# Kernel tuning notes

Measured on AMD Instinct MI355X. Metric: run time of the kernel, lower is better.

Reference implementation:

```python
import jax, jax.numpy as jnp
import numpy as np

B, F, V, E, T, NTOK, G, D = 8192, 64, 1000, 64, 2, 16, 4, 256
LN_EPS = 1e-5


def setup_inputs() -> dict:
    key = jax.random.key(0)
    ks = jax.random.split(key, 5)
    int_feats = jax.random.randint(ks[0], (B, F), 0, V, dtype=jnp.int64)
    missing_mask = jax.random.randint(ks[1], (B, F), 0, 2, dtype=jnp.int32)
    # deterministic seeded permutation of features split into NTOK equal groups
    perm = np.random.default_rng(1234).permutation(F)
    group_idx = jnp.asarray(perm.reshape(NTOK, G), dtype=jnp.int32)
    emb_tables = jax.random.normal(ks[2], (T, F, V, E), jnp.float32) * 0.02
    missing_emb = jax.random.normal(ks[3], (T, F, E), jnp.float32) * 0.02
    kW, kb = jax.random.split(ks[4])
    W = jax.random.normal(kW, (D, E * T), jnp.float32) * (1.0 / np.sqrt(E * T))
    b = jnp.zeros((D,), jnp.float32)
    ln_gamma = jnp.ones((D,), jnp.float32)
    ln_beta = jnp.zeros((D,), jnp.float32)
    return {"int_feats": int_feats, "missing_mask": missing_mask,
            "group_idx": group_idx, "emb_tables": emb_tables,
            "missing_emb": missing_emb, "W": W, "b": b,
            "ln_gamma": ln_gamma, "ln_beta": ln_beta}


def reference(int_feats, missing_mask, group_idx, emb_tables, missing_emb, W, b, ln_gamma, ln_beta):
    f_idx = jnp.arange(F)[None, :]  # (1, F) broadcast with (B, F) ids
    # per-table feature embedding gather: [T, B, F, E]
    feats = jax.vmap(lambda tbl: tbl[f_idx, int_feats])(emb_tables)
    # additive missing embeddings
    mask = missing_mask.astype(feats.dtype)
    feats = feats + mask[None, :, :, None] * missing_emb[:, None, :, :]
    # token-group mean pooling: [T, B, NTOK, G, E] -> [T, B, NTOK, E]
    pooled = feats[:, :, group_idx, :].mean(axis=3)
    # concat tables along feature dim (table order preserved): [B, NTOK, T*E]
    x = jnp.moveaxis(pooled, 0, 2).reshape(B, NTOK, T * E)
    # Linear -> SiLU -> LayerNorm
    h = jax.nn.silu(x @ W.T + b)
    mu = h.mean(-1, keepdims=True)
    var = ((h - mu) ** 2).mean(-1, keepdims=True)
    return (h - mu) * jax.lax.rsqrt(var + LN_EPS) * ln_gamma + ln_beta
```

## Files before the change

### kernel.cpp

```cpp
#include <hip/hip_runtime.h>
#include <math.h>

#define B_    8192
#define F_    64
#define V_    1000
#define E_    64
#define T_    2
#define NTOK_ 16
#define G_    4
#define D_    256
#define K_    128
#define LN_EPS 1e-5f

#define XSP   136
#define HSP   260

typedef __attribute__((ext_vector_type(8))) short  frag_ab;
typedef __attribute__((ext_vector_type(4))) float  frag_cd;

static __device__ __forceinline__ unsigned short f2bf(float f) {
    unsigned int u = __float_as_uint(f);
    u += 0x7FFFu + ((u >> 16) & 1u);
    return (unsigned short)(u >> 16);
}

__global__ __launch_bounds__(256) void convert_w_kernel(const float* __restrict__ W,
                                                        unsigned int* __restrict__ Wb_packed) {
    const int i = blockIdx.x * 256 + threadIdx.x;
    if (i < (D_ * K_) / 2) {
        const float2 v = *(const float2*)(W + (size_t)i * 2);
        Wb_packed[i] = (unsigned int)f2bf(v.x) | ((unsigned int)f2bf(v.y) << 16);
    }
}

__global__ __launch_bounds__(256) void fused_tokenizer_kernel(
    const int*   __restrict__ int_feats,
    const int*   __restrict__ missing_mask,
    const int*   __restrict__ group_idx,
    const float* __restrict__ emb_tables,
    const float* __restrict__ missing_emb,
    const unsigned short* __restrict__ Wb,
    const float* __restrict__ bias,
    const float* __restrict__ gamma,
    const float* __restrict__ beta,
    float*       __restrict__ out)
{
    __shared__ unsigned short xs[NTOK_][XSP];
    __shared__ float          hs[NTOK_][HSP];
    __shared__ int   sid[F_];
    __shared__ int   smask[F_];
    __shared__ int   sg[NTOK_ * G_];

    const int tid  = threadIdx.x;
    const int b    = blockIdx.x;
    const int lane = tid & 63;
    const int wave = tid >> 6;

    if (tid < F_) {
        sid[tid]   = int_feats[b * F_ + tid];
        smask[tid] = missing_mask[b * F_ + tid];
        sg[tid]    = group_idx[tid];
    }
    __syncthreads();

#pragma unroll
    for (int i = 0; i < 2; ++i) {
        const int c  = i * 256 + tid;
        const int n  = c >> 5;
        const int r4 = c & 31;
        const int t  = r4 >> 4;
        const int e  = (r4 & 15) * 4;
        float ax = 0.f, ay = 0.f, az = 0.f, aw = 0.f;
#pragma unroll
        for (int g = 0; g < G_; ++g) {
            const int f  = sg[n * G_ + g];
            const int id = sid[f];
            const float4 v = *(const float4*)(emb_tables + (((size_t)(t * F_ + f) * V_) + id) * E_ + e);
            float vx = v.x, vy = v.y, vz = v.z, vw = v.w;
            if (smask[f]) {
                const float4 mv = *(const float4*)(missing_emb + (size_t)(t * F_ + f) * E_ + e);
                vx += mv.x; vy += mv.y; vz += mv.z; vw += mv.w;
            }
            ax += vx; ay += vy; az += vz; aw += vw;
        }
        union { unsigned int u[2]; } pk;
        pk.u[0] = (unsigned int)f2bf(0.25f * ax) | ((unsigned int)f2bf(0.25f * ay) << 16);
        pk.u[1] = (unsigned int)f2bf(0.25f * az) | ((unsigned int)f2bf(0.25f * aw) << 16);
        *(uint2*)(&xs[n][r4 * 4]) = make_uint2(pk.u[0], pk.u[1]);
    }
    __syncthreads();

    {
        const int mA = lane & 15;
        const int q  = lane >> 4;

        frag_ab a[4];
#pragma unroll
        for (int s = 0; s < 4; ++s)
            a[s] = *(const frag_ab*)(&xs[mA][32 * s + 8 * q]);

#pragma unroll
        for (int t = 0; t < 4; ++t) {
            const int nb   = wave * 64 + t * 16;
            const int nrow = nb + mA;
            const unsigned short* wp = Wb + (size_t)nrow * K_ + 8 * q;

            frag_cd acc = {0.f, 0.f, 0.f, 0.f};
#pragma unroll
            for (int s = 0; s < 4; ++s) {
                const frag_ab bfr = *(const frag_ab*)(wp + 32 * s);
                acc = __builtin_amdgcn_mfma_f32_16x16x32_bf16(a[s], bfr, acc, 0, 0, 0);
            }
            const float bn = bias[nrow];
#pragma unroll
            for (int reg = 0; reg < 4; ++reg) {
                const int tok = q * 4 + reg;
                const float z = acc[reg] + bn;
                hs[tok][nrow] = z / (1.f + __expf(-z));
            }
        }
    }
    __syncthreads();

    {
#pragma unroll
        for (int qq = 0; qq < 4; ++qq) {
            const int n = wave * 4 + qq;
            const float4 v = *(const float4*)(&hs[n][lane * 4]);
            float s  = v.x + v.y + v.z + v.w;
            float ss = v.x * v.x + v.y * v.y + v.z * v.z + v.w * v.w;
#pragma unroll
            for (int off = 32; off > 0; off >>= 1) {
                s  += __shfl_down(s,  off, 64);
                ss += __shfl_down(ss, off, 64);
            }
            s  = __shfl(s,  0, 64);
            ss = __shfl(ss, 0, 64);
            const float mu   = s * (1.f / D_);
            const float var  = ss * (1.f / D_) - mu * mu;
            const float rsig = rsqrtf(var + LN_EPS);

            const float4 gm = *(const float4*)(gamma + lane * 4);
            const float4 bt = *(const float4*)(beta  + lane * 4);
            float4 o;
            o.x = (v.x - mu) * rsig * gm.x + bt.x;
            o.y = (v.y - mu) * rsig * gm.y + bt.y;
            o.z = (v.z - mu) * rsig * gm.z + bt.z;
            o.w = (v.w - mu) * rsig * gm.w + bt.w;
            *(float4*)(out + ((size_t)b * NTOK_ + n) * D_ + lane * 4) = o;
        }
    }
}

extern "C" void kernel_launch(void* const* d_in, const int* in_sizes, int n_in,
                              void* d_out, int out_size, void* d_ws, size_t ws_size,
                              hipStream_t stream) {
    const int*   int_feats    = (const int*)  d_in[0];
    const int*   missing_mask = (const int*)  d_in[1];
    const int*   group_idx    = (const int*)  d_in[2];
    const float* emb_tables   = (const float*)d_in[3];
    const float* missing_emb  = (const float*)d_in[4];
    const float* W            = (const float*)d_in[5];
    const float* bias         = (const float*)d_in[6];
    const float* gamma        = (const float*)d_in[7];
    const float* beta         = (const float*)d_in[8];
    float* out = (float*)d_out;

    unsigned short* Wb = (unsigned short*)d_ws;

    convert_w_kernel<<<(D_ * K_ / 2 + 255) / 256, 256, 0, stream>>>(W, (unsigned int*)Wb);
    fused_tokenizer_kernel<<<B_, 256, 0, stream>>>(
        int_feats, missing_mask, group_idx, emb_tables, missing_emb,
        Wb, bias, gamma, beta, out);
}
```

Before: 242.6 us.

## Keep SiLU outputs in registers and fuse LayerNorm stats via swapped MFMA operands

The MFMA operands are swapped so each lane holds four consecutive output columns for one token. The SiLU outputs stay in registers, and per-token sum and sum-of-squares are reduced with cross-lane shuffles plus a tiny shared partial array. This removes the 16x256 float shared staging buffer and its extra pass. The index, mask and group staging into shared memory is also replaced by direct global loads, and the missing-embedding branch becomes an unconditional multiply-add. A leftover, incomplete copy of the old kernel is left in the file but is not launched.

```diff
diff --git a/kernel.cpp b/kernel.cpp
--- a/kernel.cpp
+++ b/kernel.cpp
@@ -13,7 +13,6 @@
 #define LN_EPS 1e-5f
 
 #define XSP   136
-#define HSP   260
 
 typedef __attribute__((ext_vector_type(8))) short  frag_ab;
 typedef __attribute__((ext_vector_type(4))) float  frag_cd;
@@ -46,22 +45,16 @@
     float*       __restrict__ out)
 {
     __shared__ unsigned short xs[NTOK_][XSP];
-    __shared__ float          hs[NTOK_][HSP];
-    __shared__ int   sid[F_];
-    __shared__ int   smask[F_];
-    __shared__ int   sg[NTOK_ * G_];
+    __shared__ float ps [NTOK_][4];
+    __shared__ float pss[NTOK_][4];
 
     const int tid  = threadIdx.x;
     const int b    = blockIdx.x;
     const int lane = tid & 63;
     const int wave = tid >> 6;
 
-    if (tid < F_) {
-        sid[tid]   = int_feats[b * F_ + tid];
-        smask[tid] = missing_mask[b * F_ + tid];
-        sg[tid]    = group_idx[tid];
-    }
-    __syncthreads();
+    const int* __restrict__ feats_row = int_feats    + b * F_;
+    const int* __restrict__ mask_row  = missing_mask + b * F_;
 
 #pragma unroll
     for (int i = 0; i < 2; ++i) {
@@ -70,18 +63,20 @@
         const int r4 = c & 31;
         const int t  = r4 >> 4;
         const int e  = (r4 & 15) * 4;
+        const int4 fv = *(const int4*)(group_idx + n * G_);
+        const int fs[4] = {fv.x, fv.y, fv.z, fv.w};
         float ax = 0.f, ay = 0.f, az = 0.f, aw = 0.f;
 #pragma unroll
         for (int g = 0; g < G_; ++g) {
-            const int f  = sg[n * G_ + g];
-            const int id = sid[f];
-            const float4 v = *(const float4*)(emb_tables + (((size_t)(t * F_ + f) * V_) + id) * E_ + e);
-            float vx = v.x, vy = v.y, vz = v.z, vw = v.w;
-            if (smask[f]) {
-                const float4 mv = *(const float4*)(missing_emb + (size_t)(t * F_ + f) * E_ + e);
-                vx += mv.x; vy += mv.y; vz += mv.z; vw += mv.w;
-            }
-            ax += vx; ay += vy; az += vz; aw += vw;
+            const int f  = fs[g];
+            const int id = feats_row[f];
+            const float mk = (float)mask_row[f];
+            const float4 v  = *(const float4*)(emb_tables + (((size_t)(t * F_ + f) * V_) + id) * E_ + e);
+            const float4 mv = *(const float4*)(missing_emb + (size_t)(t * F_ + f) * E_ + e);
+            ax += v.x + mk * mv.x;
+            ay += v.y + mk * mv.y;
+            az += v.z + mk * mv.z;
+            aw += v.w + mk * mv.w;
         }
         union { unsigned int u[2]; } pk;
         pk.u[0] = (unsigned int)f2bf(0.25f * ax) | ((unsigned int)f2bf(0.25f * ay) << 16);
@@ -91,64 +86,186 @@
     __syncthreads();
 
     {
-        const int mA = lane & 15;
-        const int q  = lane >> 4;
+        const int m = lane & 15;
+        const int q = lane >> 4;
 
         frag_ab a[4];
 #pragma unroll
         for (int s = 0; s < 4; ++s)
-            a[s] = *(const frag_ab*)(&xs[mA][32 * s + 8 * q]);
-
-#pragma unroll
-        for (int t = 0; t < 4; ++t) {
-            const int nb   = wave * 64 + t * 16;
-            const int nrow = nb + mA;
+            a[s] = *(const frag_ab*)(&xs[m][32 * s + 8 * q]);
+
+        float h[4][4];
+        float s_acc = 0.f, ss_acc = 0.f;
+
+#pragma unroll
+        for (int tt = 0; tt < 4; ++tt) {
+            const int nt   = wave * 4 + tt;
+            const int nrow = nt * 16 + m;
             const unsigned short* wp = Wb + (size_t)nrow * K_ + 8 * q;
 
             frag_cd acc = {0.f, 0.f, 0.f, 0.f};
 #pragma unroll
             for (int s = 0; s < 4; ++s) {
-                const frag_ab bfr = *(const frag_ab*)(wp + 32 * s);
-                acc = __builtin_amdgcn_mfma_f32_16x16x32_bf16(a[s], bfr, acc, 0, 0, 0);
+                const frag_ab wfr = *(const frag_ab*)(wp + 32 * s);
+                acc = __builtin_amdgcn_mfma_f32_16x16x32_bf16(wfr, a[s], acc, 0, 0, 0);
             }
-            const float bn = bias[nrow];
+            const float4 bn = *(const float4*)(bias + nt * 16 + q * 4);
+            const float bnv[4] = {bn.x, bn.y, bn.z, bn.w};
 #pragma unroll
             for (int reg = 0; reg < 4; ++reg) {
-                const int tok = q * 4 + reg;
-                const float z = acc[reg] + bn;
-                hs[tok][nrow] = z / (1.f + __expf(-z));
+                const float z  = acc[reg] + bnv[reg];
+                const float hh = z / (1.f + __expf(-z));
+                h[tt][reg] = hh;
+                s_acc  += hh;
+                ss_acc += hh * hh;
             }
         }
+
+        s_acc  += __shfl_xor(s_acc,  16, 64);
+        ss_acc += __shfl_xor(ss_acc, 16, 64);
+        s_acc  += __shfl_xor(s_acc,  32, 64);
+        ss_acc += __shfl_xor(ss_acc, 32, 64);
+        if (q == 0) { ps[m][wave] = s_acc; pss[m][wave] = ss_acc; }
     }
     __syncthreads();
 
     {
-#pragma unroll
-        for (int qq = 0; qq < 4; ++qq) {
-            const int n = wave * 4 + qq;
-            const float4 v = *(const float4*)(&hs[n][lane * 4]);
-            float s  = v.x + v.y + v.z + v.w;
-            float ss = v.x * v.x + v.y * v.y + v.z * v.z + v.w * v.w;
-#pragma unroll
-            for (int off = 32; off > 0; off >>= 1) {
-                s  += __shfl_down(s,  off, 64);
-                ss += __shfl_down(ss, off, 64);
-            }
-            s  = __shfl(s,  0, 64);
-            ss = __shfl(ss, 0, 64);
-            const float mu   = s * (1.f / D_);
-            const float var  = ss * (1.f / D_) - mu * mu;
-            const float rsig = rsqrtf(var + LN_EPS);
-
-            const float4 gm = *(const float4*)(gamma + lane * 4);
-            const float4 bt = *(const float4*)(beta  + lane * 4);
-            float4 o;
-            o.x = (v.x - mu) * rsig * gm.x + bt.x;
-            o.y = (v.y - mu) * rsig * gm.y + bt.y;
-            o.z = (v.z - mu) * rsig * gm.z + bt.z;
-            o.w = (v.w - mu) * rsig * gm.w + bt.w;
-            *(float4*)(out + ((size_t)b * NTOK_ + n) * D_ + lane * 4) = o;
-        }
+        const int m = lane & 15;
+        const int q = lane >> 4;
+
+        const float4 p4  = *(const float4*)(&ps[m][0]);
+        const float4 pq4 = *(const float4*)(&pss[m][0]);
+        const float s_tot  = (p4.x  + p4.y)  + (p4.z  + p4.w);
+        const float ss_tot = (pq4.x + pq4.y) + (pq4.z + pq4.w);
+        const float mu   = s_tot * (1.f / D_);
+        const float var  = ss_tot * (1.f / D_) - mu * mu;
+        const float rsig = rsqrtf(var + LN_EPS);
+
+        float* __restrict__ orow = out + ((size_t)b * NTOK_ + m) * D_;
+
+        (void)q; (void)orow;
+    }
+
+    {
+    }
+}
+
+__global__ __launch_bounds__(256) void fused_tokenizer_kernel_v2(
+    const int*   __restrict__ int_feats,
+    const int*   __restrict__ missing_mask,
+    const int*   __restrict__ group_idx,
+    const float* __restrict__ emb_tables,
+    const float* __restrict__ missing_emb,
+    const unsigned short* __restrict__ Wb,
+    const float* __restrict__ bias,
+    const float* __restrict__ gamma,
+    const float* __restrict__ beta,
+    float*       __restrict__ out)
+{
+    __shared__ unsigned short xs[NTOK_][XSP];
+    __shared__ float ps [NTOK_][4];
+    __shared__ float pss[NTOK_][4];
+
+    const int tid  = threadIdx.x;
+    const int b    = blockIdx.x;
+    const int lane = tid & 63;
+    const int wave = tid >> 6;
+
+    const int* __restrict__ feats_row = int_feats    + b * F_;
+    const int* __restrict__ mask_row  = missing_mask + b * F_;
+
+#pragma unroll
+    for (int i = 0; i < 2; ++i) {
+        const int c  = i * 256 + tid;
+        const int n  = c >> 5;
+        const int r4 = c & 31;
+        const int t  = r4 >> 4;
+        const int e  = (r4 & 15) * 4;
+        const int4 fv = *(const int4*)(group_idx + n * G_);
+        const int fs[4] = {fv.x, fv.y, fv.z, fv.w};
+        float ax = 0.f, ay = 0.f, az = 0.f, aw = 0.f;
+#pragma unroll
+        for (int g = 0; g < G_; ++g) {
+            const int f  = fs[g];
+            const int id = feats_row[f];
+            const float mk = (float)mask_row[f];
+            const float4 v  = *(const float4*)(emb_tables + (((size_t)(t * F_ + f) * V_) + id) * E_ + e);
+            const float4 mv = *(const float4*)(missing_emb + (size_t)(t * F_ + f) * E_ + e);
+            ax += v.x + mk * mv.x;
+            ay += v.y + mk * mv.y;
+            az += v.z + mk * mv.z;
+            aw += v.w + mk * mv.w;
+        }
+        union { unsigned int u[2]; } pk;
+        pk.u[0] = (unsigned int)f2bf(0.25f * ax) | ((unsigned int)f2bf(0.25f * ay) << 16);
+        pk.u[1] = (unsigned int)f2bf(0.25f * az) | ((unsigned int)f2bf(0.25f * aw) << 16);
+        *(uint2*)(&xs[n][r4 * 4]) = make_uint2(pk.u[0], pk.u[1]);
+    }
+    __syncthreads();
+
+    const int m = lane & 15;
+    const int q = lane >> 4;
+
+    frag_ab a[4];
+#pragma unroll
+    for (int s = 0; s < 4; ++s)
+        a[s] = *(const frag_ab*)(&xs[m][32 * s + 8 * q]);
+
+    float h[4][4];
+    float s_acc = 0.f, ss_acc = 0.f;
+
+#pragma unroll
+    for (int tt = 0; tt < 4; ++tt) {
+        const int nt   = wave * 4 + tt;
+        const int nrow = nt * 16 + m;
+        const unsigned short* wp = Wb + (size_t)nrow * K_ + 8 * q;
+
+        frag_cd acc = {0.f, 0.f, 0.f, 0.f};
+#pragma unroll
+        for (int s = 0; s < 4; ++s) {
+            const frag_ab wfr = *(const frag_ab*)(wp + 32 * s);
+            acc = __builtin_amdgcn_mfma_f32_16x16x32_bf16(wfr, a[s], acc, 0, 0, 0);
+        }
+        const float4 bn = *(const float4*)(bias + nt * 16 + q * 4);
+        const float bnv[4] = {bn.x, bn.y, bn.z, bn.w};
+#pragma unroll
+        for (int reg = 0; reg < 4; ++reg) {
+            const float z  = acc[reg] + bnv[reg];
+            const float hh = z / (1.f + __expf(-z));
+            h[tt][reg] = hh;
+            s_acc  += hh;
+            ss_acc += hh * hh;
+        }
+    }
+
+    s_acc  += __shfl_xor(s_acc,  16, 64);
+    ss_acc += __shfl_xor(ss_acc, 16, 64);
+    s_acc  += __shfl_xor(s_acc,  32, 64);
+    ss_acc += __shfl_xor(ss_acc, 32, 64);
+    if (q == 0) { ps[m][wave] = s_acc; pss[m][wave] = ss_acc; }
+    __syncthreads();
+
+    const float4 p4  = *(const float4*)(&ps[m][0]);
+    const float4 pq4 = *(const float4*)(&pss[m][0]);
+    const float s_tot  = (p4.x  + p4.y)  + (p4.z  + p4.w);
+    const float ss_tot = (pq4.x + pq4.y) + (pq4.z + pq4.w);
+    const float mu   = s_tot * (1.f / D_);
+    const float var  = ss_tot * (1.f / D_) - mu * mu;
+    const float rsig = rsqrtf(var + LN_EPS);
+
+    float* __restrict__ orow = out + ((size_t)b * NTOK_ + m) * D_;
+#pragma unroll
+    for (int tt = 0; tt < 4; ++tt) {
+        const int nt  = wave * 4 + tt;
+        const int col = nt * 16 + q * 4;
+        const float4 gm = *(const float4*)(gamma + col);
+        const float4 bt = *(const float4*)(beta  + col);
+        float4 o;
+        o.x = (h[tt][0] - mu) * rsig * gm.x + bt.x;
+        o.y = (h[tt][1] - mu) * rsig * gm.y + bt.y;
+        o.z = (h[tt][2] - mu) * rsig * gm.z + bt.z;
+        o.w = (h[tt][3] - mu) * rsig * gm.w + bt.w;
+        *(float4*)(orow + col) = o;
     }
 }
 
@@ -169,7 +286,7 @@
     unsigned short* Wb = (unsigned short*)d_ws;
 
     convert_w_kernel<<<(D_ * K_ / 2 + 255) / 256, 256, 0, stream>>>(W, (unsigned int*)Wb);
-    fused_tokenizer_kernel<<<B_, 256, 0, stream>>>(
+    fused_tokenizer_kernel_v2<<<B_, 256, 0, stream>>>(
         int_feats, missing_mask, group_idx, emb_tables, missing_emb,
         Wb, bias, gamma, beta, out);
 }
```

New measurement: 256.8 us. 5.9% more time.

## Compute LayerNorm stats in MFMA registers with transposed MFMA and shared partials

Applied to the files above, without the earlier changes.

Swaps the MFMA operand order so each lane holds four consecutive output columns for one token. SiLU values then stay in registers, and per-token sum and sum-of-squares are reduced with two xor-shuffles plus a small shared-memory partial array, replacing the separate 64-lane shuffle reduction over staged values. The normalized output is written to a shared buffer that aliases the input staging buffer, then copied to global memory with coalesced stores. This aims to cut shuffle work and shared-memory footprint per block, at the cost of an extra barrier and strided float4 writes into shared memory.

```diff
diff --git a/kernel.cpp b/kernel.cpp
--- a/kernel.cpp
+++ b/kernel.cpp
@@ -45,11 +45,15 @@
     const float* __restrict__ beta,
     float*       __restrict__ out)
 {
-    __shared__ unsigned short xs[NTOK_][XSP];
-    __shared__ float          hs[NTOK_][HSP];
+    __shared__ __align__(16) char smem[NTOK_ * HSP * 4];
+    unsigned short (*xs)[XSP] = (unsigned short (*)[XSP])smem;
+    float          (*hs)[HSP] = (float (*)[HSP])smem;
+
     __shared__ int   sid[F_];
     __shared__ int   smask[F_];
     __shared__ int   sg[NTOK_ * G_];
+    __shared__ float ps [NTOK_][4];
+    __shared__ float pss[NTOK_][4];
 
     const int tid  = threadIdx.x;
     const int b    = blockIdx.x;
@@ -90,65 +94,75 @@
     }
     __syncthreads();
 
-    {
-        const int mA = lane & 15;
-        const int q  = lane >> 4;
+    const int m = lane & 15;
+    const int q = lane >> 4;
 
-        frag_ab a[4];
+    frag_ab a[4];
 #pragma unroll
-        for (int s = 0; s < 4; ++s)
-            a[s] = *(const frag_ab*)(&xs[mA][32 * s + 8 * q]);
+    for (int s = 0; s < 4; ++s)
+        a[s] = *(const frag_ab*)(&xs[m][32 * s + 8 * q]);
+
+    float h[4][4];
+    float s_acc = 0.f, ss_acc = 0.f;
 
 #pragma unroll
-        for (int t = 0; t < 4; ++t) {
-            const int nb   = wave * 64 + t * 16;
-            const int nrow = nb + mA;
-            const unsigned short* wp = Wb + (size_t)nrow * K_ + 8 * q;
+    for (int tt = 0; tt < 4; ++tt) {
+        const int nt   = wave * 4 + tt;
+        const int nrow = nt * 16 + m;
+        const unsigned short* wp = Wb + (size_t)nrow * K_ + 8 * q;
 
-            frag_cd acc = {0.f, 0.f, 0.f, 0.f};
+        frag_cd acc = {0.f, 0.f, 0.f, 0.f};
 #pragma unroll
-            for (int s = 0; s < 4; ++s) {
-                const frag_ab bfr = *(const frag_ab*)(wp + 32 * s);
-                acc = __builtin_amdgcn_mfma_f32_16x16x32_bf16(a[s], bfr, acc, 0, 0, 0);
-            }
-            const float bn = bias[nrow];
+        for (int s = 0; s < 4; ++s) {
+            const frag_ab wfr = *(const frag_ab*)(wp + 32 * s);
+            acc = __builtin_amdgcn_mfma_f32_16x16x32_bf16(wfr, a[s], acc, 0, 0, 0);
+        }
+        const float4 bn = *(const float4*)(bias + nt * 16 + q * 4);
+        const float bnv[4] = {bn.x, bn.y, bn.z, bn.w};
 #pragma unroll
-            for (int reg = 0; reg < 4; ++reg) {
-                const int tok = q * 4 + reg;
-                const float z = acc[reg] + bn;
-                hs[tok][nrow] = z / (1.f + __expf(-z));
-            }
+        for (int reg = 0; reg < 4; ++reg) {
+            const float z  = acc[reg] + bnv[reg];
+            const float hh = z / (1.f + __expf(-z));
+            h[tt][reg] = hh;
+            s_acc  += hh;
+            ss_acc += hh * hh;
         }
+    }
+
+    s_acc  += __shfl_xor(s_acc,  16, 64);
+    ss_acc += __shfl_xor(ss_acc, 16, 64);
+    s_acc  += __shfl_xor(s_acc,  32, 64);
+    ss_acc += __shfl_xor(ss_acc, 32, 64);
+    if (q == 0) { ps[m][wave] = s_acc; pss[m][wave] = ss_acc; }
+    __syncthreads();
+
+    const float4 p4  = *(const float4*)(&ps[m][0]);
+    const float4 pq4 = *(const float4*)(&pss[m][0]);
+    const float s_tot  = (p4.x  + p4.y)  + (p4.z  + p4.w);
+    const float ss_tot = (pq4.x + pq4.y) + (pq4.z + pq4.w);
+    const float mu   = s_tot * (1.f / D_);
+    const float var  = ss_tot * (1.f / D_) - mu * mu;
+    const float rsig = rsqrtf(var + LN_EPS);
+
+#pragma unroll
+    for (int tt = 0; tt < 4; ++tt) {
+        const int col = (wave * 4 + tt) * 16 + q * 4;
+        const float4 gm = *(const float4*)(gamma + col);
+        const float4 bt = *(const float4*)(beta  + col);
+        float4 o;
+        o.x = (h[tt][0] - mu) * rsig * gm.x + bt.x;
+        o.y = (h[tt][1] - mu) * rsig * gm.y + bt.y;
+        o.z = (h[tt][2] - mu) * rsig * gm.z + bt.z;
+        o.w = (h[tt][3] - mu) * rsig * gm.w + bt.w;
+        *(float4*)(&hs[m][col]) = o;
     }
     __syncthreads();
 
-    {
 #pragma unroll
-        for (int qq = 0; qq < 4; ++qq) {
-            const int n = wave * 4 + qq;
-            const float4 v = *(const float4*)(&hs[n][lane * 4]);
-            float s  = v.x + v.y + v.z + v.w;
-            float ss = v.x * v.x + v.y * v.y + v.z * v.z + v.w * v.w;
-#pragma unroll
-            for (int off = 32; off > 0; off >>= 1) {
-                s  += __shfl_down(s,  off, 64);
-                ss += __shfl_down(ss, off, 64);
-            }
-            s  = __shfl(s,  0, 64);
-            ss = __shfl(ss, 0, 64);
-            const float mu   = s * (1.f / D_);
-            const float var  = ss * (1.f / D_) - mu * mu;
-            const float rsig = rsqrtf(var + LN_EPS);
-
-            const float4 gm = *(const float4*)(gamma + lane * 4);
-            const float4 bt = *(const float4*)(beta  + lane * 4);
-            float4 o;
-            o.x = (v.x - mu) * rsig * gm.x + bt.x;
-            o.y = (v.y - mu) * rsig * gm.y + bt.y;
-            o.z = (v.z - mu) * rsig * gm.z + bt.z;
-            o.w = (v.w - mu) * rsig * gm.w + bt.w;
-            *(float4*)(out + ((size_t)b * NTOK_ + n) * D_ + lane * 4) = o;
-        }
+    for (int qq = 0; qq < 4; ++qq) {
+        const int n = wave * 4 + qq;
+        const float4 v = *(const float4*)(&hs[n][lane * 4]);
+        *(float4*)(out + ((size_t)b * NTOK_ + n) * D_ + lane * 4) = v;
     }
 }
 
```

Result: slower. 248.9 us (+2.6%).

## Process two batch rows per block, reuse W fragments, fuse LayerNorm stats into GEMM

Applied to the files above, without the earlier changes.

Each block now handles two batch rows, so every W fragment loaded is used for two MFMAs. W fragments are double-buffered across output tiles, and the x and h shared buffers are aliased to cut LDS use. LayerNorm sum and sum-of-squares are accumulated in the GEMM epilogue and reduced through shared memory, which replaces the per-token shuffle reductions. The branch on the missing mask is replaced by an unconditional load and a multiply, which adds one missing_emb load per gather. Output and W-conversion stores are nontemporal, and launch bounds request higher occupancy.

```diff
diff --git a/kernel.cpp b/kernel.cpp
--- a/kernel.cpp
+++ b/kernel.cpp
@@ -12,11 +12,14 @@
 #define K_    128
 #define LN_EPS 1e-5f
 
+#define RPB   2
+#define TOK2  (NTOK_ * RPB)
 #define XSP   136
 #define HSP   260
 
 typedef __attribute__((ext_vector_type(8))) short  frag_ab;
 typedef __attribute__((ext_vector_type(4))) float  frag_cd;
+typedef __attribute__((ext_vector_type(4))) float  f32x4;
 
 static __device__ __forceinline__ unsigned short f2bf(float f) {
     unsigned int u = __float_as_uint(f);
@@ -29,11 +32,12 @@
     const int i = blockIdx.x * 256 + threadIdx.x;
     if (i < (D_ * K_) / 2) {
         const float2 v = *(const float2*)(W + (size_t)i * 2);
-        Wb_packed[i] = (unsigned int)f2bf(v.x) | ((unsigned int)f2bf(v.y) << 16);
-    }
-}
-
-__global__ __launch_bounds__(256) void fused_tokenizer_kernel(
+        const unsigned int p = (unsigned int)f2bf(v.x) | ((unsigned int)f2bf(v.y) << 16);
+        __builtin_nontemporal_store(p, Wb_packed + i);
+    }
+}
+
+__global__ __launch_bounds__(256, 4) void fused_tokenizer_kernel(
     const int*   __restrict__ int_feats,
     const int*   __restrict__ missing_mask,
     const int*   __restrict__ group_idx,
@@ -45,110 +49,150 @@
     const float* __restrict__ beta,
     float*       __restrict__ out)
 {
-    __shared__ unsigned short xs[NTOK_][XSP];
-    __shared__ float          hs[NTOK_][HSP];
-    __shared__ int   sid[F_];
-    __shared__ int   smask[F_];
+    __shared__ __align__(16) char smem[TOK2 * HSP * 4];
+    unsigned short (*xs)[XSP] = (unsigned short (*)[XSP])smem;
+    float          (*hs)[HSP] = (float (*)[HSP])smem;
+
+    __shared__ int   sid[RPB][F_];
+    __shared__ int   smask[RPB][F_];
     __shared__ int   sg[NTOK_ * G_];
+    __shared__ float ps [TOK2][4];
+    __shared__ float pss[TOK2][4];
 
     const int tid  = threadIdx.x;
-    const int b    = blockIdx.x;
+    const int b0   = blockIdx.x * RPB;
     const int lane = tid & 63;
     const int wave = tid >> 6;
 
-    if (tid < F_) {
-        sid[tid]   = int_feats[b * F_ + tid];
-        smask[tid] = missing_mask[b * F_ + tid];
-        sg[tid]    = group_idx[tid];
-    }
-    __syncthreads();
-
-#pragma unroll
-    for (int i = 0; i < 2; ++i) {
-        const int c  = i * 256 + tid;
-        const int n  = c >> 5;
-        const int r4 = c & 31;
-        const int t  = r4 >> 4;
-        const int e  = (r4 & 15) * 4;
-        float ax = 0.f, ay = 0.f, az = 0.f, aw = 0.f;
+    if (tid < RPB * F_) {
+        const int r = tid >> 6, f = tid & 63;
+        sid[r][f]   = int_feats[(b0 + r) * F_ + f];
+        smask[r][f] = missing_mask[(b0 + r) * F_ + f];
+    }
+    if (tid < F_) sg[tid] = group_idx[tid];
+    __syncthreads();
+
+#pragma unroll
+    for (int i = 0; i < 4; ++i) {
+        const int c   = i * 256 + tid;
+        const int row = c >> 9;
+        const int cc  = c & 511;
+        const int n   = cc >> 5;
+        const int r4  = cc & 31;
+        const int t   = r4 >> 4;
+        const int e   = (r4 & 15) * 4;
+
+        float4 ev[G_], mv[G_];
+        float  mk[G_];
 #pragma unroll
         for (int g = 0; g < G_; ++g) {
             const int f  = sg[n * G_ + g];
-            const int id = sid[f];
-            const float4 v = *(const float4*)(emb_tables + (((size_t)(t * F_ + f) * V_) + id) * E_ + e);
-            float vx = v.x, vy = v.y, vz = v.z, vw = v.w;
-            if (smask[f]) {
-                const float4 mv = *(const float4*)(missing_emb + (size_t)(t * F_ + f) * E_ + e);
-                vx += mv.x; vy += mv.y; vz += mv.z; vw += mv.w;
-            }
-            ax += vx; ay += vy; az += vz; aw += vw;
+            const int id = sid[row][f];
+            ev[g] = *(const float4*)(emb_tables + (((size_t)(t * F_ + f) * V_) + id) * E_ + e);
+            mv[g] = *(const float4*)(missing_emb + (size_t)(t * F_ + f) * E_ + e);
+            mk[g] = (float)smask[row][f];
+        }
+        float ax = 0.f, ay = 0.f, az = 0.f, aw = 0.f;
+#pragma unroll
+        for (int g = 0; g < G_; ++g) {
+            ax += ev[g].x + mk[g] * mv[g].x;
+            ay += ev[g].y + mk[g] * mv[g].y;
+            az += ev[g].z + mk[g] * mv[g].z;
+            aw += ev[g].w + mk[g] * mv[g].w;
         }
         union { unsigned int u[2]; } pk;
         pk.u[0] = (unsigned int)f2bf(0.25f * ax) | ((unsigned int)f2bf(0.25f * ay) << 16);
         pk.u[1] = (unsigned int)f2bf(0.25f * az) | ((unsigned int)f2bf(0.25f * aw) << 16);
-        *(uint2*)(&xs[n][r4 * 4]) = make_uint2(pk.u[0], pk.u[1]);
-    }
-    __syncthreads();
-
+        *(uint2*)(&xs[row * NTOK_ + n][r4 * 4]) = make_uint2(pk.u[0], pk.u[1]);
+    }
+    __syncthreads();
+
+    const int m = lane & 15;
+    const int q = lane >> 4;
+
+    frag_ab a0[4], a1[4];
+#pragma unroll
+    for (int s = 0; s < 4; ++s) {
+        a0[s] = *(const frag_ab*)(&xs[m][32 * s + 8 * q]);
+        a1[s] = *(const frag_ab*)(&xs[NTOK_ + m][32 * s + 8 * q]);
+    }
+    __syncthreads();
+
+    float s0 = 0.f, ss0 = 0.f, s1 = 0.f, ss1 = 0.f;
+
+    frag_ab wb_[2][4];
     {
-        const int mA = lane & 15;
-        const int q  = lane >> 4;
-
-        frag_ab a[4];
-#pragma unroll
-        for (int s = 0; s < 4; ++s)
-            a[s] = *(const frag_ab*)(&xs[mA][32 * s + 8 * q]);
-
-#pragma unroll
-        for (int t = 0; t < 4; ++t) {
-            const int nb   = wave * 64 + t * 16;
-            const int nrow = nb + mA;
-            const unsigned short* wp = Wb + (size_t)nrow * K_ + 8 * q;
-
-            frag_cd acc = {0.f, 0.f, 0.f, 0.f};
-#pragma unroll
-            for (int s = 0; s < 4; ++s) {
-                const frag_ab bfr = *(const frag_ab*)(wp + 32 * s);
-                acc = __builtin_amdgcn_mfma_f32_16x16x32_bf16(a[s], bfr, acc, 0, 0, 0);
-            }
-            const float bn = bias[nrow];
-#pragma unroll
-            for (int reg = 0; reg < 4; ++reg) {
-                const int tok = q * 4 + reg;
-                const float z = acc[reg] + bn;
-                hs[tok][nrow] = z / (1.f + __expf(-z));
-            }
-        }
-    }
-    __syncthreads();
-
-    {
-#pragma unroll
-        for (int qq = 0; qq < 4; ++qq) {
-            const int n = wave * 4 + qq;
-            const float4 v = *(const float4*)(&hs[n][lane * 4]);
-            float s  = v.x + v.y + v.z + v.w;
-            float ss = v.x * v.x + v.y * v.y + v.z * v.z + v.w * v.w;
-#pragma unroll
-            for (int off = 32; off > 0; off >>= 1) {
-                s  += __shfl_down(s,  off, 64);
-                ss += __shfl_down(ss, off, 64);
-            }
-            s  = __shfl(s,  0, 64);
-            ss = __shfl(ss, 0, 64);
-            const float mu   = s * (1.f / D_);
-            const float var  = ss * (1.f / D_) - mu * mu;
-            const float rsig = rsqrtf(var + LN_EPS);
-
-            const float4 gm = *(const float4*)(gamma + lane * 4);
-            const float4 bt = *(const float4*)(beta  + lane * 4);
-            float4 o;
-            o.x = (v.x - mu) * rsig * gm.x + bt.x;
-            o.y = (v.y - mu) * rsig * gm.y + bt.y;
-            o.z = (v.z - mu) * rsig * gm.z + bt.z;
-            o.w = (v.w - mu) * rsig * gm.w + bt.w;
-            *(float4*)(out + ((size_t)b * NTOK_ + n) * D_ + lane * 4) = o;
-        }
+        const unsigned short* wp = Wb + (size_t)((wave * 4 + 0) * 16 + m) * K_ + 8 * q;
+#pragma unroll
+        for (int s = 0; s < 4; ++s) wb_[0][s] = *(const frag_ab*)(wp + 32 * s);
+    }
+
+#pragma unroll
+    for (int tt = 0; tt < 4; ++tt) {
+        const int cur = tt & 1;
+        if (tt < 3) {
+            const unsigned short* wp = Wb + (size_t)((wave * 4 + tt + 1) * 16 + m) * K_ + 8 * q;
+#pragma unroll
+            for (int s = 0; s < 4; ++s) wb_[cur ^ 1][s] = *(const frag_ab*)(wp + 32 * s);
+        }
+        frag_cd acc0 = {0.f, 0.f, 0.f, 0.f};
+        frag_cd acc1 = {0.f, 0.f, 0.f, 0.f};
+#pragma unroll
+        for (int s = 0; s < 4; ++s) {
+            acc0 = __builtin_amdgcn_mfma_f32_16x16x32_bf16(wb_[cur][s], a0[s], acc0, 0, 0, 0);
+            acc1 = __builtin_amdgcn_mfma_f32_16x16x32_bf16(wb_[cur][s], a1[s], acc1, 0, 0, 0);
+        }
+        const int nt  = wave * 4 + tt;
+        const int col = nt * 16 + q * 4;
+        const float4 bn = *(const float4*)(bias + col);
+        const float bnv[4] = {bn.x, bn.y, bn.z, bn.w};
+        float4 h0, h1;
+#pragma unroll
+        for (int reg = 0; reg < 4; ++reg) {
+            const float z0 = acc0[reg] + bnv[reg];
+            const float z1 = acc1[reg] + bnv[reg];
+            const float v0 = z0 / (1.f + __expf(-z0));
+            const float v1 = z1 / (1.f + __expf(-z1));
+            s0 += v0; ss0 += v0 * v0;
+            s1 += v1; ss1 += v1 * v1;
+            ((float*)&h0)[reg] = v0;
+            ((float*)&h1)[reg] = v1;
+        }
+        *(float4*)(&hs[m][col])         = h0;
+        *(float4*)(&hs[NTOK_ + m][col]) = h1;
+    }
+
+    s0  += __shfl_xor(s0,  16, 64);  ss0 += __shfl_xor(ss0, 16, 64);
+    s0  += __shfl_xor(s0,  32, 64);  ss0 += __shfl_xor(ss0, 32, 64);
+    s1  += __shfl_xor(s1,  16, 64);  ss1 += __shfl_xor(ss1, 16, 64);
+    s1  += __shfl_xor(s1,  32, 64);  ss1 += __shfl_xor(ss1, 32, 64);
+    if (q == 0) {
+        ps [m][wave] = s0;  pss[m][wave] = ss0;
+        ps [NTOK_ + m][wave] = s1;  pss[NTOK_ + m][wave] = ss1;
+    }
+    __syncthreads();
+
+    const float4 gm = *(const float4*)(gamma + lane * 4);
+    const float4 bt = *(const float4*)(beta  + lane * 4);
+#pragma unroll
+    for (int qq = 0; qq < 8; ++qq) {
+        const int n = wave * 8 + qq;
+        const float4 p4  = *(const float4*)(&ps[n][0]);
+        const float4 pq4 = *(const float4*)(&pss[n][0]);
+        const float s_tot  = (p4.x  + p4.y)  + (p4.z  + p4.w);
+        const float ss_tot = (pq4.x + pq4.y) + (pq4.z + pq4.w);
+        const float mu   = s_tot * (1.f / D_);
+        const float var  = ss_tot * (1.f / D_) - mu * mu;
+        const float rsig = rsqrtf(var + LN_EPS);
+
+        const float4 v = *(const float4*)(&hs[n][lane * 4]);
+        f32x4 o;
+        o.x = (v.x - mu) * rsig * gm.x + bt.x;
+        o.y = (v.y - mu) * rsig * gm.y + bt.y;
+        o.z = (v.z - mu) * rsig * gm.z + bt.z;
+        o.w = (v.w - mu) * rsig * gm.w + bt.w;
+        const size_t orow = ((size_t)(b0 + (n >> 4)) * NTOK_ + (n & 15)) * D_;
+        __builtin_nontemporal_store(o, (f32x4*)(out + orow + lane * 4));
     }
 }
 
@@ -169,7 +213,7 @@
     unsigned short* Wb = (unsigned short*)d_ws;
 
     convert_w_kernel<<<(D_ * K_ / 2 + 255) / 256, 256, 0, stream>>>(W, (unsigned int*)Wb);
-    fused_tokenizer_kernel<<<B_, 256, 0, stream>>>(
+    fused_tokenizer_kernel<<<B_ / RPB, 256, 0, stream>>>(
         int_feats, missing_mask, group_idx, emb_tables, missing_emb,
         Wb, bias, gamma, beta, out);
 }
```

After: 222.9 us. 8.1% less time.
